# Optimization experiments

Hardware: AMD Instinct MI355X
Metric: run time of the kernel (lower is better)

The kernel has to match this reference:

```python
import jax, jax.numpy as jnp
import numpy as np

SIZE = 512  # padded length (init kwarg `size`); also L of the input


def setup_inputs() -> dict:
    key = jax.random.key(0)
    k0, k1, k2, k3 = jax.random.split(key, 4)
    B, L, H = 4096, SIZE, 30
    x = jax.random.normal(k0, (B, 21, L), jnp.float32)
    seq_hmm = jax.random.uniform(k1, (H, L), jnp.float32)
    ss_hmm = jax.random.uniform(k2, (3, L), jnp.float32)
    W = jax.random.normal(k3, (3, 20 + H), jnp.float32) * 0.05
    b = jnp.zeros((3,), jnp.float32)
    return {"x": x, "seq_hmm": seq_hmm, "ss_hmm": ss_hmm, "W": W, "b": b}


def _pack(src, dest, size):
    # src: [C, L], dest: [L] with values in [0, size]; slot `size` is a dump
    # slot for gap columns, dropped by the final slice. Left-packs the
    # non-gap columns, exactly like hmm[i,:,:n_idx] = src[:, idx] in torch.
    C = src.shape[0]
    buf = jnp.zeros((C, size + 1), src.dtype)
    return buf.at[:, dest].set(src)[:, :size]


def reference(x, seq_hmm, ss_hmm, W, b):
    B = x.shape[0]
    size = SIZE
    x = x.reshape(B, 21, -1)                       # [B,21,L]
    mask = jnp.argmax(x, axis=1) != 0              # [B,L] non-gap positions
    ls = mask.sum(-1).astype(x.dtype)              # [B] n_idx per sample
    # destination column for each source column; gaps -> dump slot `size`
    dest = jnp.where(mask, jnp.cumsum(mask, axis=-1) - 1, size)  # [B,L]
    # source channels: x[1:] (20 aa channels) stacked with the shared profile
    src = jnp.concatenate(
        [x[:, 1:, :], jnp.broadcast_to(seq_hmm, (B,) + seq_hmm.shape)], axis=1
    )                                               # [B,20+H,L]
    hmm = jax.vmap(_pack, in_axes=(0, 0, None))(src, dest, size)       # [B,20+H,size]
    weights = jax.vmap(_pack, in_axes=(None, 0, None))(ss_hmm, dest, size)  # [B,3,size]
    # stand-in for model_ss3(hmm)[2]: 1x1 channel projection -> [B,3,size]
    logits = jnp.einsum('bcs,oc->bos', hmm, W) + b[None, :, None]
    p_ss3 = jax.nn.softmax(logits, axis=1)
    return jnp.log((weights * p_ss3).reshape(B, -1).sum(-1) / ls)
```

## Files before the change

kernel.cpp:

```cpp
#include <hip/hip_runtime.h>
#include <math.h>

#define L 512
#define NCH 21
#define H 30
#define NAA 20
#define WSTRIDE 50

__global__ void precompute_proj(const float* __restrict__ seq_hmm,
                                const float* __restrict__ W,
                                const float* __restrict__ bvec,
                                float* __restrict__ proj) {
    const int l = threadIdx.x;
    float a0 = bvec[0], a1 = bvec[1], a2 = bvec[2];
#pragma unroll
    for (int h = 0; h < H; ++h) {
        const float s = seq_hmm[h * L + l];
        a0 = fmaf(W[0 * WSTRIDE + NAA + h], s, a0);
        a1 = fmaf(W[1 * WSTRIDE + NAA + h], s, a1);
        a2 = fmaf(W[2 * WSTRIDE + NAA + h], s, a2);
    }
    proj[0 * L + l] = a0;
    proj[1 * L + l] = a1;
    proj[2 * L + l] = a2;
}

__global__ __launch_bounds__(128) void qpml_main(
        const float* __restrict__ x,
        const float* __restrict__ ss_hmm,
        const float* __restrict__ W,
        const float* __restrict__ proj,
        float* __restrict__ out) {
    const int b = blockIdx.x;
    const int t = threadIdx.x;
    const float* xb = x + (size_t)b * NCH * L;

    __shared__ float sW[3][NAA];
    if (t < 3 * NAA) ((float*)sW)[t] = W[(t / NAA) * WSTRIDE + (t % NAA)];
    __syncthreads();

    const int l0 = 4 * t;

    float xg[4];
    {
        const float4 v = *(const float4*)(xb + l0);
        xg[0] = v.x; xg[1] = v.y; xg[2] = v.z; xg[3] = v.w;
    }

    float m[4] = {-INFINITY, -INFINITY, -INFINITY, -INFINITY};
    float a[3][4];
#pragma unroll
    for (int o = 0; o < 3; ++o) {
        const float4 p = *(const float4*)(proj + o * L + l0);
        a[o][0] = p.x; a[o][1] = p.y; a[o][2] = p.z; a[o][3] = p.w;
    }

#pragma unroll
    for (int c = 1; c < NCH; ++c) {
        const float4 v = *(const float4*)(xb + c * L + l0);
        float vv[4] = {v.x, v.y, v.z, v.w};
        const float w0 = sW[0][c - 1];
        const float w1 = sW[1][c - 1];
        const float w2 = sW[2][c - 1];
#pragma unroll
        for (int j = 0; j < 4; ++j) {
            m[j] = fmaxf(m[j], vv[j]);
            a[0][j] = fmaf(w0, vv[j], a[0][j]);
            a[1][j] = fmaf(w1, vv[j], a[1][j]);
            a[2][j] = fmaf(w2, vv[j], a[2][j]);
        }
    }

    float wss[3][4];
#pragma unroll
    for (int o = 0; o < 3; ++o) {
        const float4 s = *(const float4*)(ss_hmm + o * L + l0);
        wss[o][0] = s.x; wss[o][1] = s.y; wss[o][2] = s.z; wss[o][3] = s.w;
    }

    float lsum = 0.0f;
    float lcnt = 0.0f;
#pragma unroll
    for (int j = 0; j < 4; ++j) {
        if (m[j] > xg[j]) {
            const float mm = fmaxf(a[0][j], fmaxf(a[1][j], a[2][j]));
            const float e0 = expf(a[0][j] - mm);
            const float e1 = expf(a[1][j] - mm);
            const float e2 = expf(a[2][j] - mm);
            const float inv = 1.0f / (e0 + e1 + e2);
            lsum = fmaf((wss[0][j] * e0 + wss[1][j] * e1 + wss[2][j] * e2), inv, lsum);
            lcnt += 1.0f;
        }
    }

#pragma unroll
    for (int off = 32; off >= 1; off >>= 1) {
        lsum += __shfl_down(lsum, off);
        lcnt += __shfl_down(lcnt, off);
    }

    __shared__ float s_s[2], s_c[2];
    if ((t & 63) == 0) { s_s[t >> 6] = lsum; s_c[t >> 6] = lcnt; }
    __syncthreads();
    if (t == 0) {
        const float S = s_s[0] + s_s[1];
        const float C = s_c[0] + s_c[1];
        out[b] = logf(S / C);
    }
}

extern "C" void kernel_launch(void* const* d_in, const int* in_sizes, int n_in,
                              void* d_out, int out_size, void* d_ws, size_t ws_size,
                              hipStream_t stream) {
    const float* x       = (const float*)d_in[0];
    const float* seq_hmm = (const float*)d_in[1];
    const float* ss_hmm  = (const float*)d_in[2];
    const float* W       = (const float*)d_in[3];
    const float* bvec    = (const float*)d_in[4];
    float* out = (float*)d_out;
    float* proj = (float*)d_ws;

    precompute_proj<<<1, L, 0, stream>>>(seq_hmm, W, bvec, proj);

    const int B = in_sizes[0] / (NCH * L);
    qpml_main<<<B, 128, 0, stream>>>(x, ss_hmm, W, proj, out);
}
```

Measured before the change: 248.2 us.

## Fuse profile projection into main kernel and use nontemporal loads for x

Removes the separate single-block precompute kernel and recomputes the seq_hmm projection inside every block from L2-resident seq_hmm, eliminating one launch and the serialized dependency between kernels. Loads of x are switched to nontemporal loads so the streamed input does not pollute cache that seq_hmm and ss_hmm need. The cost is redundant per-block work: 30 extra float4 loads and 360 FMAs per thread in each of the 4096 blocks.

```diff
diff --git a/kernel.cpp b/kernel.cpp
--- a/kernel.cpp
+++ b/kernel.cpp
@@ -7,79 +7,80 @@
 #define NAA 20
 #define WSTRIDE 50
 
-__global__ void precompute_proj(const float* __restrict__ seq_hmm,
-                                const float* __restrict__ W,
-                                const float* __restrict__ bvec,
-                                float* __restrict__ proj) {
-    const int l = threadIdx.x;
-    float a0 = bvec[0], a1 = bvec[1], a2 = bvec[2];
-#pragma unroll
-    for (int h = 0; h < H; ++h) {
-        const float s = seq_hmm[h * L + l];
-        a0 = fmaf(W[0 * WSTRIDE + NAA + h], s, a0);
-        a1 = fmaf(W[1 * WSTRIDE + NAA + h], s, a1);
-        a2 = fmaf(W[2 * WSTRIDE + NAA + h], s, a2);
-    }
-    proj[0 * L + l] = a0;
-    proj[1 * L + l] = a1;
-    proj[2 * L + l] = a2;
-}
+typedef float v4f __attribute__((ext_vector_type(4)));
 
-__global__ __launch_bounds__(128) void qpml_main(
+__global__ __launch_bounds__(128) void qpml_fused(
         const float* __restrict__ x,
+        const float* __restrict__ seq_hmm,
         const float* __restrict__ ss_hmm,
         const float* __restrict__ W,
-        const float* __restrict__ proj,
+        const float* __restrict__ bvec,
         float* __restrict__ out) {
     const int b = blockIdx.x;
     const int t = threadIdx.x;
     const float* xb = x + (size_t)b * NCH * L;
 
-    __shared__ float sW[3][NAA];
-    if (t < 3 * NAA) ((float*)sW)[t] = W[(t / NAA) * WSTRIDE + (t % NAA)];
+    __shared__ float sW[3][WSTRIDE];
+    __shared__ float sb[3];
+    if (t < 3 * WSTRIDE) ((float*)sW)[t] = W[t];
+    if (t < 3) sb[t] = bvec[t];
     __syncthreads();
 
     const int l0 = 4 * t;
 
-    float xg[4];
-    {
-        const float4 v = *(const float4*)(xb + l0);
-        xg[0] = v.x; xg[1] = v.y; xg[2] = v.z; xg[3] = v.w;
-    }
-
-    float m[4] = {-INFINITY, -INFINITY, -INFINITY, -INFINITY};
     float a[3][4];
 #pragma unroll
     for (int o = 0; o < 3; ++o) {
-        const float4 p = *(const float4*)(proj + o * L + l0);
-        a[o][0] = p.x; a[o][1] = p.y; a[o][2] = p.z; a[o][3] = p.w;
+        const float bo = sb[o];
+#pragma unroll
+        for (int j = 0; j < 4; ++j) a[o][j] = bo;
+    }
+
+#pragma unroll
+    for (int h = 0; h < H; ++h) {
+        const v4f s = *(const v4f*)(seq_hmm + h * L + l0);
+        const float w0 = sW[0][NAA + h];
+        const float w1 = sW[1][NAA + h];
+        const float w2 = sW[2][NAA + h];
+#pragma unroll
+        for (int j = 0; j < 4; ++j) {
+            a[0][j] = fmaf(w0, s[j], a[0][j]);
+            a[1][j] = fmaf(w1, s[j], a[1][j]);
+            a[2][j] = fmaf(w2, s[j], a[2][j]);
+        }
+    }
+
+    float xg[4], m[4];
+    {
+        const v4f v = __builtin_nontemporal_load((const v4f*)(xb + l0));
+#pragma unroll
+        for (int j = 0; j < 4; ++j) { xg[j] = v[j]; m[j] = -INFINITY; }
     }
 
 #pragma unroll
     for (int c = 1; c < NCH; ++c) {
-        const float4 v = *(const float4*)(xb + c * L + l0);
-        float vv[4] = {v.x, v.y, v.z, v.w};
+        const v4f v = __builtin_nontemporal_load((const v4f*)(xb + c * L + l0));
         const float w0 = sW[0][c - 1];
         const float w1 = sW[1][c - 1];
         const float w2 = sW[2][c - 1];
 #pragma unroll
         for (int j = 0; j < 4; ++j) {
-            m[j] = fmaxf(m[j], vv[j]);
-            a[0][j] = fmaf(w0, vv[j], a[0][j]);
-            a[1][j] = fmaf(w1, vv[j], a[1][j]);
-            a[2][j] = fmaf(w2, vv[j], a[2][j]);
+            m[j] = fmaxf(m[j], v[j]);
+            a[0][j] = fmaf(w0, v[j], a[0][j]);
+            a[1][j] = fmaf(w1, v[j], a[1][j]);
+            a[2][j] = fmaf(w2, v[j], a[2][j]);
         }
     }
 
     float wss[3][4];
 #pragma unroll
     for (int o = 0; o < 3; ++o) {
-        const float4 s = *(const float4*)(ss_hmm + o * L + l0);
-        wss[o][0] = s.x; wss[o][1] = s.y; wss[o][2] = s.z; wss[o][3] = s.w;
+        const v4f s = *(const v4f*)(ss_hmm + o * L + l0);
+#pragma unroll
+        for (int j = 0; j < 4; ++j) wss[o][j] = s[j];
     }
 
-    float lsum = 0.0f;
-    float lcnt = 0.0f;
+    float lsum = 0.0f, lcnt = 0.0f;
 #pragma unroll
     for (int j = 0; j < 4; ++j) {
         if (m[j] > xg[j]) {
@@ -88,7 +89,7 @@
             const float e1 = expf(a[1][j] - mm);
             const float e2 = expf(a[2][j] - mm);
             const float inv = 1.0f / (e0 + e1 + e2);
-            lsum = fmaf((wss[0][j] * e0 + wss[1][j] * e1 + wss[2][j] * e2), inv, lsum);
+            lsum = fmaf(wss[0][j] * e0 + wss[1][j] * e1 + wss[2][j] * e2, inv, lsum);
             lcnt += 1.0f;
         }
     }
@@ -103,9 +104,7 @@
     if ((t & 63) == 0) { s_s[t >> 6] = lsum; s_c[t >> 6] = lcnt; }
     __syncthreads();
     if (t == 0) {
-        const float S = s_s[0] + s_s[1];
-        const float C = s_c[0] + s_c[1];
-        out[b] = logf(S / C);
+        out[b] = logf((s_s[0] + s_s[1]) / (s_c[0] + s_c[1]));
     }
 }
 
@@ -118,10 +117,7 @@
     const float* W       = (const float*)d_in[3];
     const float* bvec    = (const float*)d_in[4];
     float* out = (float*)d_out;
-    float* proj = (float*)d_ws;
-
-    precompute_proj<<<1, L, 0, stream>>>(seq_hmm, W, bvec, proj);
 
     const int B = in_sizes[0] / (NCH * L);
-    qpml_main<<<B, 128, 0, stream>>>(x, ss_hmm, W, proj, out);
+    qpml_fused<<<B, 128, 0, stream>>>(x, seq_hmm, ss_hmm, W, bvec, out);
 }
```

New measurement: 258.4 us. 4.1% more time.
